# Performance work log

Hardware: AMD Instinct MI355X
Metric: run time of the kernel (lower is better)

The kernel has to match this reference:

```python
import jax, jax.numpy as jnp
import numpy as np

TILES = 8           # OpenCV createCLAHE default tileGridSize=(8,8)
CLIP_LIMIT = 1.2    # module init arg


def _clahe(img, clip_limit=CLIP_LIMIT, tiles=TILES):
    """CLAHE on a [C,H,W] float image in [0,1]; H,W divisible by `tiles`."""
    C, H, W = img.shape
    th, tw = H // tiles, W // tiles
    area = th * tw
    clip = max(int(clip_limit * area / 256.0), 1)  # OpenCV clip-limit scaling

    # Quantize to 8-bit bins (matches (img*255).astype(uint8) truncation)
    v = jnp.clip((img * 255.0).astype(jnp.int32), 0, 255)        # [C,H,W]

    # ---- per-tile, per-channel 256-bin histogram via segment_sum ----
    ty = jnp.arange(H) // th
    tx = jnp.arange(W) // tw
    tile = ty[:, None] * tiles + tx[None, :]                      # [H,W]
    seg = (jnp.arange(C)[:, None, None] * (tiles * tiles) + tile[None]) * 256 + v
    hist = jax.ops.segment_sum(
        jnp.ones((C * H * W,), jnp.float32), seg.reshape(-1),
        num_segments=C * tiles * tiles * 256,
    ).reshape(C, tiles, tiles, 256)

    # ---- clip + uniform redistribution of excess ----
    clipped = jnp.minimum(hist, jnp.float32(clip))
    excess = (hist - clipped).sum(-1, keepdims=True)
    clipped = clipped + excess / 256.0

    # ---- CDF -> per-tile LUT ----
    cdf = jnp.cumsum(clipped, axis=-1)
    lut = jnp.clip(jnp.round(cdf * (255.0 / area)), 0.0, 255.0)  # [C,T,T,256]

    # ---- bilinear interpolation between the 4 neighboring tile LUTs ----
    fy = (jnp.arange(H, dtype=jnp.float32) + 0.5) / th - 0.5
    fx = (jnp.arange(W, dtype=jnp.float32) + 0.5) / tw - 0.5
    y0 = jnp.clip(jnp.floor(fy), 0, tiles - 1).astype(jnp.int32)
    x0 = jnp.clip(jnp.floor(fx), 0, tiles - 1).astype(jnp.int32)
    ay = jnp.clip(fy - y0.astype(jnp.float32), 0.0, 1.0)
    ax = jnp.clip(fx - x0.astype(jnp.float32), 0.0, 1.0)
    y1 = jnp.minimum(y0 + 1, tiles - 1)
    x1 = jnp.minimum(x0 + 1, tiles - 1)

    ci = jnp.arange(C)[:, None, None]
    Y0, Y1 = y0[None, :, None], y1[None, :, None]
    X0, X1 = x0[None, None, :], x1[None, None, :]
    g00 = lut[ci, Y0, X0, v]
    g01 = lut[ci, Y0, X1, v]
    g10 = lut[ci, Y1, X0, v]
    g11 = lut[ci, Y1, X1, v]

    wy = ay[None, :, None]
    wx = ax[None, None, :]
    top = g00 * (1.0 - wx) + g01 * wx
    bot = g10 * (1.0 - wx) + g11 * wx
    out = top * (1.0 - wy) + bot * wy
    return (out / 255.0).astype(jnp.float32)


def setup_inputs() -> dict:
    key = jax.random.key(0)
    img = jax.random.uniform(key, (3, 4096, 4096), dtype=jnp.float32)
    return {"img": img}


def reference(img):
    # Deterministic baseline: always apply CLAHE (the p-gated identity branch
    # of the torch module is trivial and excluded for correctness testing).
    return _clahe(img)
```

## Files before the change

kernel.cpp:

```cpp
#include <hip/hip_runtime.h>
#include <stdint.h>

#define TILES 8
#define HH 4096
#define WW 4096
#define CC 3
#define TH 512
#define TW 512
#define AREA (TH * TW)
#define CLIPV 1228u

typedef float f4 __attribute__((ext_vector_type(4)));

__global__ __launch_bounds__(256) void clahe_hist_kernel(
    const float* __restrict__ img,
    uint32_t* __restrict__ vpack,
    int store_v,
    uint32_t* __restrict__ hist_part)
{
    __shared__ uint32_t sh[4 * 264];
    const int tid  = threadIdx.x;
    const int wave = tid >> 6;
    uint32_t* myh  = sh + wave * 264;

    for (int i = tid; i < 4 * 264; i += 256) sh[i] = 0;
    __syncthreads();

    const int bid = blockIdx.x;
    const int sub = bid & 15;
    const int tl  = bid >> 4;
    const int tx  = tl & 7;
    const int ty  = (tl >> 3) & 7;
    const int c   = tl >> 6;

    const size_t base4 = ((size_t)c * HH + (size_t)(ty * TH + sub * 32)) * (WW / 4)
                       + (size_t)tx * (TW / 4);
    const f4* img4 = (const f4*)img;

    for (int it = 0; it < 4; ++it) {
        const int i0 = it * 1024 + tid;
        size_t addr[4];
        f4 p[4];
#pragma unroll
        for (int j = 0; j < 4; ++j) {
            const int s  = i0 + j * 256;
            const int rl = s >> 7;
            const int c4 = s & 127;
            addr[j] = base4 + (size_t)rl * (WW / 4) + (size_t)c4;
            p[j] = __builtin_nontemporal_load(&img4[addr[j]]);
        }
#pragma unroll
        for (int j = 0; j < 4; ++j) {
            int v0 = min(max((int)(p[j][0] * 255.0f), 0), 255);
            int v1 = min(max((int)(p[j][1] * 255.0f), 0), 255);
            int v2 = min(max((int)(p[j][2] * 255.0f), 0), 255);
            int v3 = min(max((int)(p[j][3] * 255.0f), 0), 255);

            atomicAdd(&myh[v0], 1u);
            atomicAdd(&myh[v1], 1u);
            atomicAdd(&myh[v2], 1u);
            atomicAdd(&myh[v3], 1u);

            if (store_v) {
                uint32_t pk = (uint32_t)v0 | ((uint32_t)v1 << 8) |
                              ((uint32_t)v2 << 16) | ((uint32_t)v3 << 24);
                vpack[addr[j]] = pk;
            }
        }
    }
    __syncthreads();

    const uint32_t s = sh[tid] + sh[264 + tid] + sh[528 + tid] + sh[792 + tid];
    hist_part[(size_t)bid * 256 + tid] = s;
}

__global__ __launch_bounds__(256) void clahe_lut_kernel(
    const uint32_t* __restrict__ hist_part,
    float* __restrict__ lut)
{
    __shared__ uint32_t exs[4];
    __shared__ float wsum[4];

    const int tid  = threadIdx.x;
    const int wave = tid >> 6;
    const int lane = tid & 63;
    const int blk  = blockIdx.x;

    const uint32_t* hp = hist_part + (size_t)blk * 16 * 256;
    uint32_t h = 0;
#pragma unroll
    for (int s = 0; s < 16; ++s) h += hp[s * 256 + tid];

    const uint32_t cl = min(h, CLIPV);
    uint32_t ex = h - cl;

#pragma unroll
    for (int d = 32; d > 0; d >>= 1) ex += __shfl_down(ex, d, 64);
    if (lane == 0) exs[wave] = ex;
    __syncthreads();
    const uint32_t extot = exs[0] + exs[1] + exs[2] + exs[3];

    float x = (float)cl + (float)extot * (1.0f / 256.0f);

#pragma unroll
    for (int d = 1; d < 64; d <<= 1) {
        float t = __shfl_up(x, d, 64);
        if (lane >= d) x += t;
    }
    if (lane == 63) wsum[wave] = x;
    __syncthreads();
    float add = 0.0f;
    for (int w = 0; w < wave; ++w) add += wsum[w];
    const float cdf = x + add;

    float l = rintf(cdf * (255.0f / (float)AREA));
    l = fminf(fmaxf(l, 0.0f), 255.0f);
    lut[(size_t)blk * 256 + tid] = l;
}

__global__ __launch_bounds__(256) void clahe_apply_kernel(
    const float* __restrict__ img,
    const uint32_t* __restrict__ vpack,
    const float* __restrict__ lut,
    float* __restrict__ out,
    int use_v)
{
    __shared__ float rb[TILES * 256];

    const int tid = threadIdx.x;
    const int b = blockIdx.x;
    const int y = b & (HH - 1);
    const int c = b >> 12;

    const size_t rowbase4 = ((size_t)c * HH + (size_t)y) * (WW / 4);
    const f4* img4 = (const f4*)img;

    uint32_t pv[4];
    f4 p[4];
    if (use_v) {
#pragma unroll
        for (int s = 0; s < 4; ++s) pv[s] = vpack[rowbase4 + s * 256 + tid];
    } else {
#pragma unroll
        for (int s = 0; s < 4; ++s) p[s] = img4[rowbase4 + s * 256 + tid];
    }

    const float fy = ((float)y + 0.5f) * (1.0f / (float)TH) - 0.5f;
    int y0 = (int)floorf(fy);
    y0 = min(max(y0, 0), TILES - 1);
    const float ay = fminf(fmaxf(fy - (float)y0, 0.0f), 1.0f);
    const int y1 = min(y0 + 1, TILES - 1);

    const float* lr0 = lut + ((size_t)(c * TILES + y0) * TILES) * 256;
    const float* lr1 = lut + ((size_t)(c * TILES + y1) * TILES) * 256;

#pragma unroll
    for (int k = 0; k < 8; ++k) {
        const int i = k * 256 + tid;
        const float a = lr0[i];
        const float d = lr1[i];
        rb[i] = a + ay * (d - a);
    }
    __syncthreads();

#pragma unroll
    for (int s = 0; s < 4; ++s) {
        const int slot = s * 256 + tid;

        const int xbase = slot * 4;
        const float fx0 = ((float)xbase + 0.5f) * (1.0f / (float)TW) - 0.5f;
        int x0 = (int)floorf(fx0);
        x0 = min(max(x0, 0), TILES - 1);
        const int x1 = min(x0 + 1, TILES - 1);
        const float* r0 = rb + x0 * 256;
        const float* r1 = rb + x1 * 256;
        const float fxr = fx0 - (float)x0;

        float res[4];
#pragma unroll
        for (int k = 0; k < 4; ++k) {
            int v;
            if (use_v) {
                v = (int)((pv[s] >> (8 * k)) & 255u);
            } else {
                v = min(max((int)(p[s][k] * 255.0f), 0), 255);
            }
            const float ax = fminf(fmaxf(fxr + (float)k * (1.0f / (float)TW), 0.0f), 1.0f);
            const float g0 = r0[v];
            const float g1 = r1[v];
            res[k] = (g0 + ax * (g1 - g0)) * (1.0f / 255.0f);
        }
        f4 o4 = { res[0], res[1], res[2], res[3] };
        __builtin_nontemporal_store(o4, ((f4*)out) + rowbase4 + slot);
    }
}

extern "C" void kernel_launch(void* const* d_in, const int* in_sizes, int n_in,
                              void* d_out, int out_size, void* d_ws, size_t ws_size,
                              hipStream_t stream)
{
    const float* img = (const float*)d_in[0];
    float* out = (float*)d_out;

    uint8_t* ws = (uint8_t*)d_ws;
    float*    lut       = (float*)ws;
    uint32_t* hist_part = (uint32_t*)(ws + 196608);
    uint32_t* vpack     = (uint32_t*)(ws + 196608 + 3145728);

    const size_t need_v = 196608 + 3145728 + (size_t)CC * HH * WW;
    const int use_v = (ws_size >= need_v) ? 1 : 0;

    clahe_hist_kernel<<<CC * 64 * 16, 256, 0, stream>>>(img, vpack, use_v, hist_part);
    clahe_lut_kernel<<<CC * 64, 256, 0, stream>>>(hist_part, lut);
    clahe_apply_kernel<<<CC * HH, 256, 0, stream>>>(img, vpack, lut, out, use_v);
}
```

Before: 335.4 us.

## Restructure apply kernel into tile-quadrant blocks with interleaved LUT pairs

The apply kernel now launches one block per 64-row strip inside each tile instead of one block per full image row. Each block stages only the four neighbouring LUTs it needs into shared memory, interleaving left and right entries so each lookup is a single 8-byte read. The full bilinear interpolation is done per pixel, and eight loads are batched per iteration to keep more memory traffic in flight. This replaces the per-row staging of 8 vertically interpolated LUTs (2048 global reads per row) with far fewer LUT loads per block. In exchange there are fewer, longer blocks, more ALU work per pixel, and some shared-memory bank conflicts from the random gathers.

```diff
diff --git a/kernel.cpp b/kernel.cpp
--- a/kernel.cpp
+++ b/kernel.cpp
@@ -11,6 +11,7 @@
 #define CLIPV 1228u
 
 typedef float f4 __attribute__((ext_vector_type(4)));
+typedef float f2 __attribute__((ext_vector_type(2)));
 
 __global__ __launch_bounds__(256) void clahe_hist_kernel(
     const float* __restrict__ img,
@@ -125,73 +126,88 @@
     float* __restrict__ out,
     int use_v)
 {
-    __shared__ float rb[TILES * 256];
+    __shared__ float Lh[4 * 512];
 
     const int tid = threadIdx.x;
-    const int b = blockIdx.x;
-    const int y = b & (HH - 1);
-    const int c = b >> 12;
-
-    const size_t rowbase4 = ((size_t)c * HH + (size_t)y) * (WW / 4);
+    const int bid = blockIdx.x;
+    const int sub = bid & 7;
+    const int tl  = bid >> 3;
+    const int tx  = tl & 7;
+    const int ty  = (tl >> 3) & 7;
+    const int c   = tl >> 6;
+
+    const int row0 = ty * TH + sub * 64;
+    const size_t base4 = ((size_t)c * HH + (size_t)row0) * (WW / 4) + (size_t)tx * (TW / 4);
+
+    const int y0 = (sub < 4) ? max(ty - 1, 0) : ty;
+    const int y1 = min(y0 + 1, TILES - 1);
+    const int xl = max(tx - 1, 0);
+    const int xr = min(tx + 1, TILES - 1);
+
+#pragma unroll
+    for (int t = 0; t < 8; ++t) {
+        const int e   = t * 256 + tid;
+        const int arr = e >> 9;
+        const int i   = e & 511;
+        const int v   = i >> 1;
+        const int w   = i & 1;
+        const int ys  = (arr & 2) ? y1 : y0;
+        const int xs  = (arr & 1) ? (w ? xr : tx) : (w ? tx : xl);
+        Lh[e] = lut[((size_t)(c * TILES + ys) * TILES + xs) * 256 + v];
+    }
+    __syncthreads();
+
+    const int c4 = tid & 127;
+    const float fx0 = ((float)(tx * TW + c4 * 4) + 0.5f) * (1.0f / (float)TW) - 0.5f;
+    int x0i = (int)floorf(fx0);
+    x0i = min(max(x0i, 0), TILES - 1);
+    const float fxr = fx0 - (float)x0i;
+    float ax[4];
+#pragma unroll
+    for (int k = 0; k < 4; ++k)
+        ax[k] = fminf(fmaxf(fxr + (float)k * (1.0f / (float)TW), 0.0f), 1.0f);
+
+    const int x0k = (c4 < 64) ? 0 : 1;
+    const float* topA = Lh + x0k * 512;
+    const float* botA = Lh + 1024 + x0k * 512;
+    const float y0f = (float)y0;
+
     const f4* img4 = (const f4*)img;
-
-    uint32_t pv[4];
-    f4 p[4];
-    if (use_v) {
-#pragma unroll
-        for (int s = 0; s < 4; ++s) pv[s] = vpack[rowbase4 + s * 256 + tid];
-    } else {
-#pragma unroll
-        for (int s = 0; s < 4; ++s) p[s] = img4[rowbase4 + s * 256 + tid];
-    }
-
-    const float fy = ((float)y + 0.5f) * (1.0f / (float)TH) - 0.5f;
-    int y0 = (int)floorf(fy);
-    y0 = min(max(y0, 0), TILES - 1);
-    const float ay = fminf(fmaxf(fy - (float)y0, 0.0f), 1.0f);
-    const int y1 = min(y0 + 1, TILES - 1);
-
-    const float* lr0 = lut + ((size_t)(c * TILES + y0) * TILES) * 256;
-    const float* lr1 = lut + ((size_t)(c * TILES + y1) * TILES) * 256;
-
-#pragma unroll
-    for (int k = 0; k < 8; ++k) {
-        const int i = k * 256 + tid;
-        const float a = lr0[i];
-        const float d = lr1[i];
-        rb[i] = a + ay * (d - a);
-    }
-    __syncthreads();
-
-#pragma unroll
-    for (int s = 0; s < 4; ++s) {
-        const int slot = s * 256 + tid;
-
-        const int xbase = slot * 4;
-        const float fx0 = ((float)xbase + 0.5f) * (1.0f / (float)TW) - 0.5f;
-        int x0 = (int)floorf(fx0);
-        x0 = min(max(x0, 0), TILES - 1);
-        const int x1 = min(x0 + 1, TILES - 1);
-        const float* r0 = rb + x0 * 256;
-        const float* r1 = rb + x1 * 256;
-        const float fxr = fx0 - (float)x0;
-
-        float res[4];
-#pragma unroll
-        for (int k = 0; k < 4; ++k) {
-            int v;
-            if (use_v) {
-                v = (int)((pv[s] >> (8 * k)) & 255u);
-            } else {
-                v = min(max((int)(p[s][k] * 255.0f), 0), 255);
+    f4* out4 = (f4*)out;
+
+    for (int it8 = 0; it8 < 4; ++it8) {
+        uint32_t pv[8];
+        f4 p[8];
+        int rls[8];
+        size_t off[8];
+#pragma unroll
+        for (int j = 0; j < 8; ++j) {
+            const int s = (it8 * 8 + j) * 256 + tid;
+            const int rl = s >> 7;
+            rls[j] = rl;
+            off[j] = (size_t)rl * (WW / 4) + (size_t)c4;
+            if (use_v) pv[j] = vpack[base4 + off[j]];
+            else       p[j]  = __builtin_nontemporal_load(&img4[base4 + off[j]]);
+        }
+#pragma unroll
+        for (int j = 0; j < 8; ++j) {
+            const float fy = ((float)(row0 + rls[j]) + 0.5f) * (1.0f / (float)TH) - 0.5f;
+            const float ay = fminf(fmaxf(fy - y0f, 0.0f), 1.0f);
+            float res[4];
+#pragma unroll
+            for (int k = 0; k < 4; ++k) {
+                int v;
+                if (use_v) v = (int)((pv[j] >> (8 * k)) & 255u);
+                else       v = min(max((int)(p[j][k] * 255.0f), 0), 255);
+                const f2 tpr = *(const f2*)&topA[v * 2];
+                const f2 bpr = *(const f2*)&botA[v * 2];
+                const float top = tpr[0] + ax[k] * (tpr[1] - tpr[0]);
+                const float bot = bpr[0] + ax[k] * (bpr[1] - bpr[0]);
+                res[k] = (top + ay * (bot - top)) * (1.0f / 255.0f);
             }
-            const float ax = fminf(fmaxf(fxr + (float)k * (1.0f / (float)TW), 0.0f), 1.0f);
-            const float g0 = r0[v];
-            const float g1 = r1[v];
-            res[k] = (g0 + ax * (g1 - g0)) * (1.0f / 255.0f);
-        }
-        f4 o4 = { res[0], res[1], res[2], res[3] };
-        __builtin_nontemporal_store(o4, ((f4*)out) + rowbase4 + slot);
+            f4 o = { res[0], res[1], res[2], res[3] };
+            __builtin_nontemporal_store(o, &out4[base4 + off[j]]);
+        }
     }
 }
 
@@ -212,5 +228,5 @@
 
     clahe_hist_kernel<<<CC * 64 * 16, 256, 0, stream>>>(img, vpack, use_v, hist_part);
     clahe_lut_kernel<<<CC * 64, 256, 0, stream>>>(hist_part, lut);
-    clahe_apply_kernel<<<CC * HH, 256, 0, stream>>>(img, vpack, lut, out, use_v);
-}
+    clahe_apply_kernel<<<CC * TILES * TILES * 8, 256, 0, stream>>>(img, vpack, lut, out, use_v);
+}
```

New measurement: 345.4 us. 1.03x slower.
